# Kernel optimization log

Hardware: AMD Instinct MI355X
Metric: run time of the kernel (lower is better)

The kernel has to match this reference:

```python
import jax, jax.numpy as jnp
import numpy as np
from jax import lax

# Model dims (see init_kwargs / mamba_ssm defaults)
B_, L_, D_IN = 8, 512, 128
D_MODEL, N_LAYERS = 512, 2
EXPAND, D_STATE, D_CONV = 2, 16, 4
D_INNER = EXPAND * D_MODEL          # 1024
DT_RANK = (D_MODEL + 15) // 16      # 32


def setup_inputs() -> dict:
    key = jax.random.key(0)
    ks = iter(jax.random.split(key, 32))
    def p(shape, scale=0.02):
        return jax.random.normal(next(ks), shape, jnp.float32) * scale
    inp = {}
    inp["x"] = jax.random.normal(next(ks), (B_, L_, D_IN), jnp.float32)
    # input projection (Linear(input_dim, d_model), with bias)
    inp["proj_in_w"] = p((D_MODEL, D_IN))
    inp["proj_in_b"] = p((D_MODEL,))
    # stacked per-layer Mamba params (leading dim = N_LAYERS)
    inp["in_proj_w"] = p((N_LAYERS, 2 * D_INNER, D_MODEL))      # no bias (mamba default)
    inp["conv_w"]    = p((N_LAYERS, D_INNER, D_CONV))           # depthwise conv1d
    inp["conv_b"]    = p((N_LAYERS, D_INNER))
    inp["x_proj_w"]  = p((N_LAYERS, DT_RANK + 2 * D_STATE, D_INNER))
    inp["dt_proj_w"] = p((N_LAYERS, D_INNER, DT_RANK))
    inp["dt_proj_b"] = jnp.full((N_LAYERS, D_INNER), 0.1, jnp.float32)
    inp["A_log"]     = jnp.log(jnp.tile(jnp.arange(1, D_STATE + 1, dtype=jnp.float32), (N_LAYERS, D_INNER, 1)))
    inp["Dm"]        = jnp.ones((N_LAYERS, D_INNER), jnp.float32)
    inp["out_proj_w"] = p((N_LAYERS, D_MODEL, D_INNER))         # no bias
    # classifier head: Linear(d_model, 64) -> ReLU -> Linear(64, 1)
    inp["cls_w1"] = p((64, D_MODEL)); inp["cls_b1"] = p((64,))
    inp["cls_w2"] = p((1, 64));       inp["cls_b2"] = p((1,))
    return inp


def _mamba_block(h, in_w, cw, cb, xp_w, dt_w, dt_b, A_log, Dm, out_w):
    B, L, _ = h.shape
    xz = jnp.einsum('bld,ed->ble', h, in_w)           # (B, L, 2*d_inner)
    xi, z = jnp.split(xz, 2, axis=-1)
    # causal depthwise conv1d (pad left d_conv-1, crop to L)
    xc = xi.transpose(0, 2, 1)                         # (B, d_inner, L)
    xc = lax.conv_general_dilated(
        xc, cw[:, None, :], (1,), [(D_CONV - 1, 0)],
        feature_group_count=D_INNER,
        dimension_numbers=('NCH', 'OIH', 'NCH')) + cb[None, :, None]
    xc = jax.nn.silu(xc).transpose(0, 2, 1)            # (B, L, d_inner)
    x_dbl = jnp.einsum('bld,ed->ble', xc, xp_w)        # (B, L, dt_rank + 2*d_state)
    dt, Bm, Cm = jnp.split(x_dbl, [DT_RANK, DT_RANK + D_STATE], axis=-1)
    dt = jax.nn.softplus(jnp.einsum('blr,dr->bld', dt, dt_w) + dt_b)  # (B, L, d_inner)
    A = -jnp.exp(A_log)                                # (d_inner, d_state)

    def step(hst, ins):
        dt_t, B_t, C_t, x_t = ins                      # (B,di),(B,ds),(B,ds),(B,di)
        dA = jnp.exp(dt_t[..., None] * A)              # (B, di, ds)
        hst = dA * hst + (dt_t * x_t)[..., None] * B_t[:, None, :]
        y = jnp.einsum('bds,bs->bd', hst, C_t)
        return hst, y

    h0 = jnp.zeros((B, D_INNER, D_STATE), h.dtype)
    xs = (dt.transpose(1, 0, 2), Bm.transpose(1, 0, 2),
          Cm.transpose(1, 0, 2), xc.transpose(1, 0, 2))
    _, ys = lax.scan(step, h0, xs)                     # ys: (L, B, d_inner)
    y = ys.transpose(1, 0, 2) + xc * Dm                # skip term D*x
    y = y * jax.nn.silu(z)                             # gate
    return jnp.einsum('ble,de->bld', y, out_w)         # (B, L, d_model)


def reference(x, proj_in_w, proj_in_b, in_proj_w, conv_w, conv_b, x_proj_w,
              dt_proj_w, dt_proj_b, A_log, Dm, out_proj_w,
              cls_w1, cls_b1, cls_w2, cls_b2):
    h = jnp.einsum('bli,di->bld', x, proj_in_w) + proj_in_b
    for l in range(N_LAYERS):
        h = _mamba_block(h, in_proj_w[l], conv_w[l], conv_b[l], x_proj_w[l],
                         dt_proj_w[l], dt_proj_b[l], A_log[l], Dm[l], out_proj_w[l])
    h = h.mean(axis=1)                                 # (B, d_model); dropout = identity (eval)
    h = jax.nn.relu(h @ cls_w1.T + cls_b1)
    logits = (h @ cls_w2.T + cls_b2).squeeze(-1)       # (B,)
    return logits
```

## Files before the change

### kernel.cpp

```cpp
#include <hip/hip_runtime.h>
#include <hip/hip_bf16.h>

#define B_   8
#define L_   512
#define DIN  128
#define DM   512
#define NLAY 2
#define DI   1024
#define DS   16
#define DTR  32
#define BL   (B_ * L_)
#define KS   8
#define CL   128
#define NCH  (L_ / CL)

typedef short bf16x8 __attribute__((ext_vector_type(8)));
typedef float floatx4 __attribute__((ext_vector_type(4)));

__device__ __forceinline__ unsigned short f2bf(float f) {
    unsigned int u = __float_as_uint(f);
    unsigned int r = (u + 0x7FFF + ((u >> 16) & 1)) >> 16;
    return (unsigned short)r;
}
__device__ __forceinline__ float bf2f(unsigned short u) {
    return __uint_as_float((unsigned int)u << 16);
}

#if __has_builtin(__builtin_amdgcn_exp2f)
#define EXP2(x) __builtin_amdgcn_exp2f(x)
#else
#define EXP2(x) __expf((x) * 0.69314718056f)
#endif

__global__ __launch_bounds__(256) void cvt_all(
    const float* __restrict__ x,  unsigned short* __restrict__ xbf,
    const float* __restrict__ pw, unsigned short* __restrict__ wpin,
    const float* __restrict__ iw, unsigned short* __restrict__ win,
    const float* __restrict__ ow, unsigned short* __restrict__ wout,
    float* __restrict__ hm)
{
    int bid = blockIdx.x;
    if (bid >= 1824) {
        int i = (bid - 1824) * 2048 + threadIdx.x * 8;
        float4 z = make_float4(0.f, 0.f, 0.f, 0.f);
        *(float4*)(hm + i) = z;
        *(float4*)(hm + i + 4) = z;
        return;
    }
    const float* src; unsigned short* dst; int off;
    if      (bid < 256)  { src = x;  dst = xbf;  off = bid; }
    else if (bid < 288)  { src = pw; dst = wpin; off = bid - 256; }
    else if (bid < 1312) { src = iw; dst = win;  off = bid - 288; }
    else                 { src = ow; dst = wout; off = bid - 1312; }
    int i = (off * 256 + threadIdx.x) * 8;
    float4 a = *(const float4*)(src + i);
    float4 b = *(const float4*)(src + i + 4);
    unsigned short o[8];
    o[0] = f2bf(a.x); o[1] = f2bf(a.y); o[2] = f2bf(a.z); o[3] = f2bf(a.w);
    o[4] = f2bf(b.x); o[5] = f2bf(b.y); o[6] = f2bf(b.z); o[7] = f2bf(b.w);
    *(uint4*)(dst + i) = *(uint4*)o;
}

__global__ __launch_bounds__(256) void gemm_mfma(
    const unsigned short* __restrict__ A,
    const unsigned short* __restrict__ W,
    float* __restrict__ C, unsigned short* __restrict__ Cb,
    int N, int K)
{
    __shared__ unsigned short As[128 * 40];
    __shared__ unsigned short Ws[128 * 40];

    const int tid  = threadIdx.x;
    const int row  = tid >> 1;
    const int half = tid & 1;
    const long aBase = (long)(blockIdx.y * 128 + row) * K + half * 16;
    const long wBase = (long)(blockIdx.x * 128 + row) * K + half * 16;
    const int  lbase = row * 40 + half * 16;

    const int lane = tid & 63;
    const int wv   = tid >> 6;
    const int wm   = (wv >> 1) * 64;
    const int wn   = (wv & 1) * 64;
    const int lr   = lane & 15;
    const int q    = lane >> 4;

    floatx4 acc[4][4];
#pragma unroll
    for (int i = 0; i < 4; ++i)
#pragma unroll
        for (int j = 0; j < 4; ++j)
#pragma unroll
            for (int r = 0; r < 4; ++r) acc[i][j][r] = 0.f;

    for (int k0 = 0; k0 < K; k0 += 32) {
        __syncthreads();
        const unsigned short* ap = A + aBase + k0;
        const unsigned short* wp = W + wBase + k0;
        uint4 a0 = *(const uint4*)ap;
        uint4 a1 = *(const uint4*)(ap + 8);
        uint4 w0 = *(const uint4*)wp;
        uint4 w1 = *(const uint4*)(wp + 8);
        *(uint4*)(As + lbase)     = a0;
        *(uint4*)(As + lbase + 8) = a1;
        *(uint4*)(Ws + lbase)     = w0;
        *(uint4*)(Ws + lbase + 8) = w1;
        __syncthreads();

        bf16x8 af[4], bfr[4];
#pragma unroll
        for (int i = 0; i < 4; ++i)
            af[i] = *(const bf16x8*)(As + (wm + i * 16 + lr) * 40 + q * 8);
#pragma unroll
        for (int j = 0; j < 4; ++j)
            bfr[j] = *(const bf16x8*)(Ws + (wn + j * 16 + lr) * 40 + q * 8);
#pragma unroll
        for (int i = 0; i < 4; ++i)
#pragma unroll
            for (int j = 0; j < 4; ++j)
                acc[i][j] = __builtin_amdgcn_mfma_f32_16x16x32_bf16(
                    af[i], bfr[j], acc[i][j], 0, 0, 0);
    }

#pragma unroll
    for (int i = 0; i < 4; ++i) {
#pragma unroll
        for (int r = 0; r < 4; ++r) {
            const int  crow = blockIdx.y * 128 + wm + i * 16 + q * 4 + r;
            const long base = (long)crow * N + blockIdx.x * 128 + wn + lr;
#pragma unroll
            for (int j = 0; j < 4; ++j) {
                float v = acc[i][j][r];
                if (C)  C[base + j * 16] = v;
                if (Cb) Cb[base + j * 16] = f2bf(v);
            }
        }
    }
}

__global__ __launch_bounds__(256) void gemm_mfma_n64(
    const unsigned short* __restrict__ A,
    const unsigned short* __restrict__ W,
    const float* __restrict__ bias,
    float* __restrict__ C, unsigned short* __restrict__ Cb,
    int N, int K, int meanmode, float* __restrict__ hm)
{
    __shared__ unsigned short As[128 * 40];
    __shared__ unsigned short Ws[64 * 40];
    __shared__ float colsum[64];

    const int tid   = threadIdx.x;
    const int arow  = tid >> 1;
    const int ahalf = tid & 1;
    const long aBase = (long)(blockIdx.y * 128 + arow) * K + ahalf * 16;
    const int  albase = arow * 40 + ahalf * 16;
    const int wrow = tid >> 2;
    const int wq   = tid & 3;
    const long wBase = (long)(blockIdx.x * 64 + wrow) * K + wq * 8;
    const int  wlbase = wrow * 40 + wq * 8;

    const int lane = tid & 63;
    const int wv   = tid >> 6;
    const int wm   = wv * 32;
    const int lr   = lane & 15;
    const int q    = lane >> 4;

    floatx4 acc[2][4];
#pragma unroll
    for (int i = 0; i < 2; ++i)
#pragma unroll
        for (int j = 0; j < 4; ++j)
#pragma unroll
            for (int r = 0; r < 4; ++r) acc[i][j][r] = 0.f;

    for (int k0 = 0; k0 < K; k0 += 32) {
        __syncthreads();
        const unsigned short* ap = A + aBase + k0;
        uint4 a0 = *(const uint4*)ap;
        uint4 a1 = *(const uint4*)(ap + 8);
        uint4 w0 = *(const uint4*)(W + wBase + k0);
        *(uint4*)(As + albase)     = a0;
        *(uint4*)(As + albase + 8) = a1;
        *(uint4*)(Ws + wlbase)     = w0;
        __syncthreads();

        bf16x8 af[2], bfr[4];
#pragma unroll
        for (int i = 0; i < 2; ++i)
            af[i] = *(const bf16x8*)(As + (wm + i * 16 + lr) * 40 + q * 8);
#pragma unroll
        for (int j = 0; j < 4; ++j)
            bfr[j] = *(const bf16x8*)(Ws + (j * 16 + lr) * 40 + q * 8);
#pragma unroll
        for (int i = 0; i < 2; ++i)
#pragma unroll
            for (int j = 0; j < 4; ++j)
                acc[i][j] = __builtin_amdgcn_mfma_f32_16x16x32_bf16(
                    af[i], bfr[j], acc[i][j], 0, 0, 0);
    }

    if (meanmode) {
        if (tid < 64) colsum[tid] = 0.f;
        __syncthreads();
#pragma unroll
        for (int j = 0; j < 4; ++j) {
            float p = 0.f;
#pragma unroll
            for (int i = 0; i < 2; ++i)
#pragma unroll
                for (int r = 0; r < 4; ++r) p += acc[i][j][r];
            atomicAdd(&colsum[j * 16 + lr], p);
        }
        __syncthreads();
        if (tid < 64) {
            const int b = blockIdx.y >> 2;
            atomicAdd(&hm[b * DM + blockIdx.x * 64 + tid],
                      colsum[tid] * (1.f / (float)L_));
        }
        return;
    }

    float bj[4] = {0.f, 0.f, 0.f, 0.f};
    if (bias) {
#pragma unroll
        for (int j = 0; j < 4; ++j)
            bj[j] = bias[blockIdx.x * 64 + j * 16 + lr];
    }
#pragma unroll
    for (int i = 0; i < 2; ++i) {
#pragma unroll
        for (int r = 0; r < 4; ++r) {
            const int  crow = blockIdx.y * 128 + wm + i * 16 + q * 4 + r;
            const long base = (long)crow * N + blockIdx.x * 64 + lr;
#pragma unroll
            for (int j = 0; j < 4; ++j) {
                float v = acc[i][j][r] + bj[j];
                if (C)  C[base + j * 16] = v;
                if (Cb) Cb[base + j * 16] = f2bf(v);
            }
        }
    }
}

__global__ __launch_bounds__(256) void xprojconv(
    const unsigned short* __restrict__ xzb, const float* __restrict__ cw,
    const float* __restrict__ cb, const float* __restrict__ W,
    float* __restrict__ P, float* __restrict__ xcout)
{
    __shared__ float As[16][68];
    __shared__ float Ws[16][68];

    const int tid  = threadIdx.x;
    const int tx   = tid & 15;
    const int ty   = tid >> 4;
    const int lrow = tid >> 2;
    const int lk   = (tid & 3) << 2;
    const int kbase = blockIdx.x * (DI / KS);

    const int m = blockIdx.y * 64 + lrow;
    const int t = m & (L_ - 1);
    const float* Wp = W + lrow * DI + kbase + lk;

    float acc[4][4] = {};

    for (int k0 = 0; k0 < DI / KS; k0 += 16) {
        const int dcol = kbase + k0 + lk;
        float4 cbv = *(const float4*)(cb + dcol);
        float sums[4] = {cbv.x, cbv.y, cbv.z, cbv.w};
        float4 cwq[4];
#pragma unroll
        for (int q = 0; q < 4; ++q) cwq[q] = *(const float4*)(cw + (dcol + q) * 4);
#pragma unroll
        for (int w = 0; w < 4; ++w) {
            int tw = t - 3 + w;
            if (tw >= 0) {
                const uint2 up = *(const uint2*)(xzb + (long)(m - 3 + w) * (2 * DI) + dcol);
                float x0 = __uint_as_float(up.x << 16);
                float x1 = __uint_as_float(up.x & 0xffff0000u);
                float x2 = __uint_as_float(up.y << 16);
                float x3 = __uint_as_float(up.y & 0xffff0000u);
                sums[0] += ((const float*)&cwq[0])[w] * x0;
                sums[1] += ((const float*)&cwq[1])[w] * x1;
                sums[2] += ((const float*)&cwq[2])[w] * x2;
                sums[3] += ((const float*)&cwq[3])[w] * x3;
            }
        }
        float4 a4;
#pragma unroll
        for (int q = 0; q < 4; ++q)
            ((float*)&a4)[q] = sums[q] / (1.f + __expf(-sums[q]));
        float4 wv = *(const float4*)(Wp + k0);
        *(float4*)(xcout + (long)m * DI + dcol) = a4;

        __syncthreads();
        As[lk + 0][lrow] = a4.x; As[lk + 1][lrow] = a4.y;
        As[lk + 2][lrow] = a4.z; As[lk + 3][lrow] = a4.w;
        Ws[lk + 0][lrow] = wv.x; Ws[lk + 1][lrow] = wv.y;
        Ws[lk + 2][lrow] = wv.z; Ws[lk + 3][lrow] = wv.w;
        __syncthreads();
#pragma unroll
        for (int k = 0; k < 16; ++k) {
            const float4 a44 = *(const float4*)&As[k][ty << 2];
            const float4 w4  = *(const float4*)&Ws[k][tx << 2];
            acc[0][0] += a44.x * w4.x; acc[0][1] += a44.x * w4.y;
            acc[0][2] += a44.x * w4.z; acc[0][3] += a44.x * w4.w;
            acc[1][0] += a44.y * w4.x; acc[1][1] += a44.y * w4.y;
            acc[1][2] += a44.y * w4.z; acc[1][3] += a44.y * w4.w;
            acc[2][0] += a44.z * w4.x; acc[2][1] += a44.z * w4.y;
            acc[2][2] += a44.z * w4.z; acc[2][3] += a44.z * w4.w;
            acc[3][0] += a44.w * w4.x; acc[3][1] += a44.w * w4.y;
            acc[3][2] += a44.w * w4.z; acc[3][3] += a44.w * w4.w;
        }
    }

    float* out = P + (long)blockIdx.x * (BL * 64)
               + (blockIdx.y * 64 + (ty << 2)) * 64 + (tx << 2);
#pragma unroll
    for (int i = 0; i < 4; ++i)
        *(float4*)(out + i * 64) = make_float4(acc[i][0], acc[i][1],
                                               acc[i][2], acc[i][3]);
}

__global__ __launch_bounds__(256) void xproj_reduce(
    const float* __restrict__ P, float* __restrict__ xdbl)
{
    int i = (blockIdx.x * 256 + threadIdx.x) * 4;
    float4 s = *(const float4*)(P + i);
#pragma unroll
    for (int k = 1; k < KS; ++k) {
        float4 p = *(const float4*)(P + (long)k * (BL * 64) + i);
        s.x += p.x; s.y += p.y; s.z += p.z; s.w += p.w;
    }
    *(float4*)(xdbl + i) = s;
}

template <int CTRL>
__device__ __forceinline__ float dpp_shr_add(float v) {
    int sh = __builtin_amdgcn_update_dpp(0, __float_as_int(v), CTRL, 0xF, 0xF, true);
    return v + __int_as_float(sh);
}

__global__ __launch_bounds__(256) void scan_fused(
    const float* __restrict__ xc, const float* __restrict__ xdbl,
    const float* __restrict__ A_log, const float* __restrict__ dtw,
    const float* __restrict__ dtpb, const float* __restrict__ Dm,
    const unsigned short* __restrict__ xzb, unsigned short* __restrict__ ysb16)
{
    __shared__ float  sdtw[16][36];
    __shared__ float  sxd [CL][36];
    __shared__ float4 sdp [CL / 2][17];
    __shared__ float4 sbc4[CL / 2][17];
    __shared__ float  sy  [16][CL + 4];

    const int tid  = threadIdx.x;
    const int s    = tid & 15;
    const int grp  = tid >> 4;
    const int bd0  = blockIdx.x * 16;
    const int b    = bd0 >> 10;
    const int d0   = bd0 & (DI - 1);
    const int mb0  = b * L_;

    const int j  = tid & 15;
    const int tt = tid >> 4;

    {
        float2 w = *(const float2*)(dtw + (d0 + j) * DTR + tt * 2);
        sdtw[j][tt * 2] = w.x; sdtw[j][tt * 2 + 1] = w.y;
    }
    const float a    = -__expf(A_log[(d0 + grp) * DS + s]);
    const float bias = dtpb[d0 + j];
    const float dmv  = Dm[d0 + j];

    float  rxc[8], rB[8], rC[8], rz[8];
    float2 rxd[8];
#pragma unroll
    for (int i = 0; i < 8; ++i) {
        int m = mb0 + tt + 16 * i;
        rxc[i] = xc[m * DI + d0 + j];
        rxd[i] = *(const float2*)(xdbl + m * 64 + j * 2);
        rB[i]  = xdbl[m * 64 + DTR + j];
        rC[i]  = xdbl[m * 64 + DTR + DS + j];
        rz[i]  = bf2f(xzb[(long)m * (2 * DI) + DI + d0 + j]);
    }

    float state = 0.f;

    for (int c = 0; c < NCH; ++c) {
        const int mbase = mb0 + c * CL;
        float xcur[8], zcur[8];
#pragma unroll
        for (int i = 0; i < 8; ++i) { xcur[i] = rxc[i]; zcur[i] = rz[i]; }

        __syncthreads();
#pragma unroll
        for (int i = 0; i < 8; ++i) {
            int t = tt + 16 * i;
            *(float2*)&sxd[t][j * 2] = rxd[i];
            ((float2*)&sbc4[t >> 1][j])[t & 1] = make_float2(rB[i], rC[i]);
        }
        __syncthreads();

        if (c < NCH - 1) {
#pragma unroll
            for (int i = 0; i < 8; ++i) {
                int m = mbase + CL + tt + 16 * i;
                rxc[i] = xc[m * DI + d0 + j];
                rxd[i] = *(const float2*)(xdbl + m * 64 + j * 2);
                rB[i]  = xdbl[m * 64 + DTR + j];
                rC[i]  = xdbl[m * 64 + DTR + DS + j];
                rz[i]  = bf2f(xzb[(long)m * (2 * DI) + DI + d0 + j]);
            }
        }

        {
            float4 wreg[8];
#pragma unroll
            for (int k = 0; k < 8; ++k) wreg[k] = *(const float4*)&sdtw[j][k * 4];
#pragma unroll
            for (int i = 0; i < 8; ++i) {
                int t = tt + 16 * i;
                float acc = bias;
#pragma unroll
                for (int k = 0; k < 8; ++k) {
                    float4 xv = *(const float4*)&sxd[t][k * 4];
                    acc += xv.x * wreg[k].x + xv.y * wreg[k].y
                         + xv.z * wreg[k].z + xv.w * wreg[k].w;
                }
                float dt = (acc > 20.f) ? acc : __logf(1.f + __expf(acc));
                ((float2*)&sdp[t >> 1][j])[t & 1] =
                    make_float2(dt * 1.44269504f, dt * xcur[i]);
            }
        }
        __syncthreads();

        for (int t4 = 0; t4 < CL; t4 += 4) {
            float ybuf[4];
#pragma unroll
            for (int h = 0; h < 2; ++h) {
                const int t2 = (t4 >> 1) + h;
                const float4 dp = sdp[t2][grp];
                const float4 bc = sbc4[t2][s];
                {
                    const float dA = EXP2(dp.x * a);
                    state = fmaf(dA, state, dp.y * bc.x);
                    float contrib = state * bc.y;
                    contrib = dpp_shr_add<0x111>(contrib);
                    contrib = dpp_shr_add<0x112>(contrib);
                    contrib = dpp_shr_add<0x114>(contrib);
                    contrib = dpp_shr_add<0x118>(contrib);
                    ybuf[h * 2] = contrib;
                }
                {
                    const float dA = EXP2(dp.z * a);
                    state = fmaf(dA, state, dp.w * bc.z);
                    float contrib = state * bc.w;
                    contrib = dpp_shr_add<0x111>(contrib);
                    contrib = dpp_shr_add<0x112>(contrib);
                    contrib = dpp_shr_add<0x114>(contrib);
                    contrib = dpp_shr_add<0x118>(contrib);
                    ybuf[h * 2 + 1] = contrib;
                }
            }
            if (s == 15) *(float4*)&sy[grp][t4] = *(float4*)ybuf;
        }
        __syncthreads();

#pragma unroll
        for (int i = 0; i < 8; ++i) {
            int t = tt + 16 * i;
            float z = zcur[i];
            float sz = z / (1.f + __expf(-z));
            float val = (sy[j][t] + xcur[i] * dmv) * sz;
            ysb16[(mbase + t) * DI + d0 + j] = f2bf(val);
        }
    }
}

__global__ __launch_bounds__(512) void meancls_kernel(
    const float* __restrict__ hm, const float* __restrict__ w1,
    const float* __restrict__ b1, const float* __restrict__ w2,
    const float* __restrict__ b2, float* __restrict__ out)
{
    __shared__ float shm[DM];
    __shared__ float su[64];
    const int b = blockIdx.x, tid = threadIdx.x;
    shm[tid] = hm[b * DM + tid];
    __syncthreads();

    const int j = tid >> 3, sl = tid & 7;
    const float* wr = w1 + j * DM + sl * 64;
    const float* hb = shm + sl * 64;
    float p = 0.f;
    for (int k = 0; k < 64; k += 4)
        p += hb[k] * wr[k] + hb[k+1] * wr[k+1]
           + hb[k+2] * wr[k+2] + hb[k+3] * wr[k+3];
    p += __shfl_xor(p, 1);
    p += __shfl_xor(p, 2);
    p += __shfl_xor(p, 4);
    if (sl == 0) su[j] = fmaxf(p + b1[j], 0.f) * w2[j];
    __syncthreads();
    if (tid < 64) {
        float v = su[tid];
#pragma unroll
        for (int off = 32; off; off >>= 1) v += __shfl_down(v, off);
        if (tid == 0) out[b] = v + b2[0];
    }
}

extern "C" void kernel_launch(void* const* d_in, const int* in_sizes, int n_in,
                              void* d_out, int out_size, void* d_ws, size_t ws_size,
                              hipStream_t stream) {
    const float* x          = (const float*)d_in[0];
    const float* proj_in_w  = (const float*)d_in[1];
    const float* proj_in_b  = (const float*)d_in[2];
    const float* in_proj_w  = (const float*)d_in[3];
    const float* conv_w     = (const float*)d_in[4];
    const float* conv_b     = (const float*)d_in[5];
    const float* x_proj_w   = (const float*)d_in[6];
    const float* dt_proj_w  = (const float*)d_in[7];
    const float* dt_proj_b  = (const float*)d_in[8];
    const float* A_log      = (const float*)d_in[9];
    const float* Dm         = (const float*)d_in[10];
    const float* out_proj_w = (const float*)d_in[11];
    const float* cls_w1     = (const float*)d_in[12];
    const float* cls_b1     = (const float*)d_in[13];
    const float* cls_w2     = (const float*)d_in[14];
    const float* cls_b2     = (const float*)d_in[15];
    float* out = (float*)d_out;

    float* ws   = (float*)d_ws;
    float* h    = ws;
    float* xzf  = h    + BL * DM;
    float* xcb  = xzf  + BL * 2 * DI;
    float* xdbl = xcb  + BL * DI;
    float* scr  = xdbl + BL * 64;
    float* hm   = scr  + 2 * BL * DI;
    float* hmp  = hm   + B_ * DM;
    unsigned short* xzb  = (unsigned short*)xzf;
    unsigned short* u16  = (unsigned short*)(hmp + 64 * DM);
    unsigned short* xbf  = u16;
    unsigned short* hbf  = xbf  + BL * DIN;
    unsigned short* ysbf = hbf  + BL * DM;
    unsigned short* wpin = ysbf + BL * DI;
    unsigned short* win  = wpin + DM * DIN;
    unsigned short* wout = win  + NLAY * 2 * DI * DM;
    float* xpart = scr;

    cvt_all<<<1826, 256, 0, stream>>>(x, xbf, proj_in_w, wpin,
                                      in_proj_w, win, out_proj_w, wout, hm);

    gemm_mfma_n64<<<dim3(DM / 64, BL / 128), 256, 0, stream>>>(
        xbf, wpin, proj_in_b, nullptr, hbf, DM, DIN, 0, nullptr);

    for (int l = 0; l < NLAY; ++l) {
        gemm_mfma<<<dim3(2 * DI / 128, BL / 128), 256, 0, stream>>>(
            hbf, win + l * 2 * DI * DM, nullptr, xzb, 2 * DI, DM);
        xprojconv<<<dim3(KS, BL / 64), 256, 0, stream>>>(
            xzb, conv_w + l * DI * 4, conv_b + l * DI,
            x_proj_w + l * 64 * DI, xpart, xcb);
        xproj_reduce<<<(BL * 64) / 1024, 256, 0, stream>>>(xpart, xdbl);
        scan_fused<<<(B_ * DI) / 16, 256, 0, stream>>>(
            xcb, xdbl, A_log + l * DI * DS, dt_proj_w + l * DI * DTR,
            dt_proj_b + l * DI, Dm + l * DI, xzb, ysbf);
        if (l == NLAY - 1) {
            gemm_mfma_n64<<<dim3(DM / 64, BL / 128), 256, 0, stream>>>(
                ysbf, wout + l * DM * DI, nullptr, nullptr, nullptr,
                DM, DI, 1, hm);
        } else {
            gemm_mfma_n64<<<dim3(DM / 64, BL / 128), 256, 0, stream>>>(
                ysbf, wout + l * DM * DI, nullptr, nullptr, hbf,
                DM, DI, 0, nullptr);
        }
    }

    meancls_kernel<<<B_, 512, 0, stream>>>(hm, cls_w1, cls_b1,
                                           cls_w2, cls_b2, out);
}
```

Baseline: 347.0 us.

## Fuse classifier into last out-proj GEMM and software-pipeline scan loads

The final out-projection GEMM now ends with a last-block-done counter: the final block to finish reads the accumulated mean and runs the classifier head, which removes a separate kernel launch. The scan kernel keeps the dt_proj weights in registers instead of shared memory. Its inner loop also prefetches the next step's shared-memory operands and computes four state updates before the 16-lane DPP reductions, so reductions overlap the serial recurrence. The cost is a global atomic counter, a serial classifier tail on one block, and higher register pressure in the scan.

```diff
diff --git a/kernel.cpp b/kernel.cpp
--- a/kernel.cpp
+++ b/kernel.cpp
@@ -32,19 +32,33 @@
 #define EXP2(x) __expf((x) * 0.69314718056f)
 #endif
 
-__global__ __launch_bounds__(256) void cvt_all(
+template <int CTRL>
+__device__ __forceinline__ float dpp_shr_add(float v) {
+    int sh = __builtin_amdgcn_update_dpp(0, __float_as_int(v), CTRL, 0xF, 0xF, true);
+    return v + __int_as_float(sh);
+}
+__device__ __forceinline__ float red16(float c) {
+    c = dpp_shr_add<0x111>(c);
+    c = dpp_shr_add<0x112>(c);
+    c = dpp_shr_add<0x114>(c);
+    c = dpp_shr_add<0x118>(c);
+    return c;
+}
+
+__global__ __launch_bounds__(256) void k_cvt(
     const float* __restrict__ x,  unsigned short* __restrict__ xbf,
     const float* __restrict__ pw, unsigned short* __restrict__ wpin,
     const float* __restrict__ iw, unsigned short* __restrict__ win,
     const float* __restrict__ ow, unsigned short* __restrict__ wout,
-    float* __restrict__ hm)
+    float* __restrict__ hm, unsigned int* __restrict__ cnt)
 {
-    int bid = blockIdx.x;
+    int bid = blockIdx.x, tid = threadIdx.x;
     if (bid >= 1824) {
-        int i = (bid - 1824) * 2048 + threadIdx.x * 8;
+        int i = (bid - 1824) * 2048 + tid * 8;
         float4 z = make_float4(0.f, 0.f, 0.f, 0.f);
         *(float4*)(hm + i) = z;
         *(float4*)(hm + i + 4) = z;
+        if (bid == 1825 && tid == 0) cnt[0] = 0u;
         return;
     }
     const float* src; unsigned short* dst; int off;
@@ -52,7 +66,7 @@
     else if (bid < 288)  { src = pw; dst = wpin; off = bid - 256; }
     else if (bid < 1312) { src = iw; dst = win;  off = bid - 288; }
     else                 { src = ow; dst = wout; off = bid - 1312; }
-    int i = (off * 256 + threadIdx.x) * 8;
+    int i = (off * 256 + tid) * 8;
     float4 a = *(const float4*)(src + i);
     float4 b = *(const float4*)(src + i + 4);
     unsigned short o[8];
@@ -61,20 +75,219 @@
     *(uint4*)(dst + i) = *(uint4*)o;
 }
 
-__global__ __launch_bounds__(256) void gemm_mfma(
+__global__ __launch_bounds__(256) void k_gemm_n64(
     const unsigned short* __restrict__ A,
     const unsigned short* __restrict__ W,
-    float* __restrict__ C, unsigned short* __restrict__ Cb,
-    int N, int K)
+    const float* __restrict__ bias,
+    unsigned short* __restrict__ Cb, int K)
+{
+    __shared__ unsigned short As[128 * 40];
+    __shared__ unsigned short Ws[64 * 40];
+
+    const int tid   = threadIdx.x;
+    const int bxx   = blockIdx.x, byy = blockIdx.y;
+    const int arow  = tid >> 1;
+    const int ahalf = tid & 1;
+    const long aBase = (long)(byy * 128 + arow) * K + ahalf * 16;
+    const int  albase = arow * 40 + ahalf * 16;
+    const int wrow = tid >> 2;
+    const int wq   = tid & 3;
+    const long wBase = (long)(bxx * 64 + wrow) * K + wq * 8;
+    const int  wlbase = wrow * 40 + wq * 8;
+
+    const int lane = tid & 63;
+    const int wv   = tid >> 6;
+    const int wm   = wv * 32;
+    const int lr   = lane & 15;
+    const int q    = lane >> 4;
+
+    floatx4 acc[2][4];
+#pragma unroll
+    for (int i = 0; i < 2; ++i)
+#pragma unroll
+        for (int j = 0; j < 4; ++j)
+#pragma unroll
+            for (int r = 0; r < 4; ++r) acc[i][j][r] = 0.f;
+
+    for (int k0 = 0; k0 < K; k0 += 32) {
+        __syncthreads();
+        const unsigned short* ap = A + aBase + k0;
+        uint4 a0 = *(const uint4*)ap;
+        uint4 a1 = *(const uint4*)(ap + 8);
+        uint4 w0 = *(const uint4*)(W + wBase + k0);
+        *(uint4*)(As + albase)     = a0;
+        *(uint4*)(As + albase + 8) = a1;
+        *(uint4*)(Ws + wlbase)     = w0;
+        __syncthreads();
+
+        bf16x8 af[2], bfr[4];
+#pragma unroll
+        for (int i = 0; i < 2; ++i)
+            af[i] = *(const bf16x8*)(As + (wm + i * 16 + lr) * 40 + q * 8);
+#pragma unroll
+        for (int j = 0; j < 4; ++j)
+            bfr[j] = *(const bf16x8*)(Ws + (j * 16 + lr) * 40 + q * 8);
+#pragma unroll
+        for (int i = 0; i < 2; ++i)
+#pragma unroll
+            for (int j = 0; j < 4; ++j)
+                acc[i][j] = __builtin_amdgcn_mfma_f32_16x16x32_bf16(
+                    af[i], bfr[j], acc[i][j], 0, 0, 0);
+    }
+
+    float bj[4] = {0.f, 0.f, 0.f, 0.f};
+    if (bias) {
+#pragma unroll
+        for (int j = 0; j < 4; ++j)
+            bj[j] = bias[bxx * 64 + j * 16 + lr];
+    }
+#pragma unroll
+    for (int i = 0; i < 2; ++i) {
+#pragma unroll
+        for (int r = 0; r < 4; ++r) {
+            const int  crow = byy * 128 + wm + i * 16 + q * 4 + r;
+            const long base = (long)crow * DM + bxx * 64 + lr;
+#pragma unroll
+            for (int j = 0; j < 4; ++j)
+                Cb[base + j * 16] = f2bf(acc[i][j][r] + bj[j]);
+        }
+    }
+}
+
+__global__ __launch_bounds__(256) void k_outproj_cls(
+    const unsigned short* __restrict__ A,
+    const unsigned short* __restrict__ W,
+    float* __restrict__ hm, unsigned int* __restrict__ cnt,
+    const float* __restrict__ w1, const float* __restrict__ b1,
+    const float* __restrict__ w2, const float* __restrict__ b2,
+    float* __restrict__ out)
+{
+    __shared__ unsigned short As[128 * 40];
+    __shared__ unsigned short Ws[64 * 40];
+    __shared__ float colsum[64];
+    __shared__ int last;
+
+    const int tid = threadIdx.x;
+    const int bxx = blockIdx.x, byy = blockIdx.y;
+    const int K = DI;
+    const int arow  = tid >> 1;
+    const int ahalf = tid & 1;
+    const long aBase = (long)(byy * 128 + arow) * K + ahalf * 16;
+    const int  albase = arow * 40 + ahalf * 16;
+    const int wrow = tid >> 2;
+    const int wq   = tid & 3;
+    const long wBase = (long)(bxx * 64 + wrow) * K + wq * 8;
+    const int  wlbase = wrow * 40 + wq * 8;
+
+    const int lane = tid & 63;
+    const int wv   = tid >> 6;
+    const int wm   = wv * 32;
+    const int lr   = lane & 15;
+    const int q    = lane >> 4;
+
+    floatx4 acc[2][4];
+#pragma unroll
+    for (int i = 0; i < 2; ++i)
+#pragma unroll
+        for (int j = 0; j < 4; ++j)
+#pragma unroll
+            for (int r = 0; r < 4; ++r) acc[i][j][r] = 0.f;
+
+    for (int k0 = 0; k0 < K; k0 += 32) {
+        __syncthreads();
+        const unsigned short* ap = A + aBase + k0;
+        uint4 a0 = *(const uint4*)ap;
+        uint4 a1 = *(const uint4*)(ap + 8);
+        uint4 w0 = *(const uint4*)(W + wBase + k0);
+        *(uint4*)(As + albase)     = a0;
+        *(uint4*)(As + albase + 8) = a1;
+        *(uint4*)(Ws + wlbase)     = w0;
+        __syncthreads();
+
+        bf16x8 af[2], bfr[4];
+#pragma unroll
+        for (int i = 0; i < 2; ++i)
+            af[i] = *(const bf16x8*)(As + (wm + i * 16 + lr) * 40 + q * 8);
+#pragma unroll
+        for (int j = 0; j < 4; ++j)
+            bfr[j] = *(const bf16x8*)(Ws + (j * 16 + lr) * 40 + q * 8);
+#pragma unroll
+        for (int i = 0; i < 2; ++i)
+#pragma unroll
+            for (int j = 0; j < 4; ++j)
+                acc[i][j] = __builtin_amdgcn_mfma_f32_16x16x32_bf16(
+                    af[i], bfr[j], acc[i][j], 0, 0, 0);
+    }
+
+    __syncthreads();
+    if (tid < 64) colsum[tid] = 0.f;
+    __syncthreads();
+#pragma unroll
+    for (int j = 0; j < 4; ++j) {
+        float pp = 0.f;
+#pragma unroll
+        for (int i = 0; i < 2; ++i)
+#pragma unroll
+            for (int r = 0; r < 4; ++r) pp += acc[i][j][r];
+        atomicAdd(&colsum[j * 16 + lr], pp);
+    }
+    __syncthreads();
+    if (tid < 64) {
+        const int b = byy >> 2;
+        atomicAdd(&hm[b * DM + bxx * 64 + tid],
+                  colsum[tid] * (1.f / (float)L_));
+    }
+    __syncthreads();
+
+    if (tid == 0) {
+        __threadfence();
+        unsigned int old = atomicAdd(cnt, 1u);
+        last = (old == 255u) ? 1 : 0;
+    }
+    __syncthreads();
+    if (!last) return;
+
+    float* shm = (float*)As;
+    float* su  = (float*)Ws;
+    for (int b = 0; b < B_; ++b) {
+        shm[tid]       = atomicAdd(&hm[b * DM + tid], 0.f);
+        shm[tid + 256] = atomicAdd(&hm[b * DM + tid + 256], 0.f);
+        __syncthreads();
+        const int jj = tid >> 2, sl = tid & 3;
+        const float* wr = w1 + jj * DM + sl * 128;
+        const float* hb = shm + sl * 128;
+        float pp = 0.f;
+        for (int k = 0; k < 128; k += 4)
+            pp += hb[k] * wr[k] + hb[k+1] * wr[k+1]
+                + hb[k+2] * wr[k+2] + hb[k+3] * wr[k+3];
+        pp += __shfl_xor(pp, 1);
+        pp += __shfl_xor(pp, 2);
+        if (sl == 0) su[jj] = fmaxf(pp + b1[jj], 0.f) * w2[jj];
+        __syncthreads();
+        if (tid < 64) {
+            float v = su[tid];
+#pragma unroll
+            for (int off = 32; off; off >>= 1) v += __shfl_down(v, off);
+            if (tid == 0) out[b] = v + b2[0];
+        }
+        __syncthreads();
+    }
+}
+
+__global__ __launch_bounds__(256) void k_gemm_128(
+    const unsigned short* __restrict__ A,
+    const unsigned short* __restrict__ W,
+    unsigned short* __restrict__ Cb, int N, int K)
 {
     __shared__ unsigned short As[128 * 40];
     __shared__ unsigned short Ws[128 * 40];
 
     const int tid  = threadIdx.x;
+    const int bxx  = blockIdx.x, byy = blockIdx.y;
     const int row  = tid >> 1;
     const int half = tid & 1;
-    const long aBase = (long)(blockIdx.y * 128 + row) * K + half * 16;
-    const long wBase = (long)(blockIdx.x * 128 + row) * K + half * 16;
+    const long aBase = (long)(byy * 128 + row) * K + half * 16;
+    const long wBase = (long)(bxx * 128 + row) * K + half * 16;
     const int  lbase = row * 40 + half * 16;
 
     const int lane = tid & 63;
@@ -125,123 +338,16 @@
     for (int i = 0; i < 4; ++i) {
 #pragma unroll
         for (int r = 0; r < 4; ++r) {
-            const int  crow = blockIdx.y * 128 + wm + i * 16 + q * 4 + r;
-            const long base = (long)crow * N + blockIdx.x * 128 + wn + lr;
-#pragma unroll
-            for (int j = 0; j < 4; ++j) {
-                float v = acc[i][j][r];
-                if (C)  C[base + j * 16] = v;
-                if (Cb) Cb[base + j * 16] = f2bf(v);
-            }
-        }
-    }
-}
-
-__global__ __launch_bounds__(256) void gemm_mfma_n64(
-    const unsigned short* __restrict__ A,
-    const unsigned short* __restrict__ W,
-    const float* __restrict__ bias,
-    float* __restrict__ C, unsigned short* __restrict__ Cb,
-    int N, int K, int meanmode, float* __restrict__ hm)
-{
-    __shared__ unsigned short As[128 * 40];
-    __shared__ unsigned short Ws[64 * 40];
-    __shared__ float colsum[64];
-
-    const int tid   = threadIdx.x;
-    const int arow  = tid >> 1;
-    const int ahalf = tid & 1;
-    const long aBase = (long)(blockIdx.y * 128 + arow) * K + ahalf * 16;
-    const int  albase = arow * 40 + ahalf * 16;
-    const int wrow = tid >> 2;
-    const int wq   = tid & 3;
-    const long wBase = (long)(blockIdx.x * 64 + wrow) * K + wq * 8;
-    const int  wlbase = wrow * 40 + wq * 8;
-
-    const int lane = tid & 63;
-    const int wv   = tid >> 6;
-    const int wm   = wv * 32;
-    const int lr   = lane & 15;
-    const int q    = lane >> 4;
-
-    floatx4 acc[2][4];
-#pragma unroll
-    for (int i = 0; i < 2; ++i)
-#pragma unroll
-        for (int j = 0; j < 4; ++j)
-#pragma unroll
-            for (int r = 0; r < 4; ++r) acc[i][j][r] = 0.f;
-
-    for (int k0 = 0; k0 < K; k0 += 32) {
-        __syncthreads();
-        const unsigned short* ap = A + aBase + k0;
-        uint4 a0 = *(const uint4*)ap;
-        uint4 a1 = *(const uint4*)(ap + 8);
-        uint4 w0 = *(const uint4*)(W + wBase + k0);
-        *(uint4*)(As + albase)     = a0;
-        *(uint4*)(As + albase + 8) = a1;
-        *(uint4*)(Ws + wlbase)     = w0;
-        __syncthreads();
-
-        bf16x8 af[2], bfr[4];
-#pragma unroll
-        for (int i = 0; i < 2; ++i)
-            af[i] = *(const bf16x8*)(As + (wm + i * 16 + lr) * 40 + q * 8);
-#pragma unroll
-        for (int j = 0; j < 4; ++j)
-            bfr[j] = *(const bf16x8*)(Ws + (j * 16 + lr) * 40 + q * 8);
-#pragma unroll
-        for (int i = 0; i < 2; ++i)
+            const int  crow = byy * 128 + wm + i * 16 + q * 4 + r;
+            const long base = (long)crow * N + bxx * 128 + wn + lr;
 #pragma unroll
             for (int j = 0; j < 4; ++j)
-                acc[i][j] = __builtin_amdgcn_mfma_f32_16x16x32_bf16(
-                    af[i], bfr[j], acc[i][j], 0, 0, 0);
-    }
-
-    if (meanmode) {
-        if (tid < 64) colsum[tid] = 0.f;
-        __syncthreads();
-#pragma unroll
-        for (int j = 0; j < 4; ++j) {
-            float p = 0.f;
-#pragma unroll
-            for (int i = 0; i < 2; ++i)
-#pragma unroll
-                for (int r = 0; r < 4; ++r) p += acc[i][j][r];
-            atomicAdd(&colsum[j * 16 + lr], p);
-        }
-        __syncthreads();
-        if (tid < 64) {
-            const int b = blockIdx.y >> 2;
-            atomicAdd(&hm[b * DM + blockIdx.x * 64 + tid],
-                      colsum[tid] * (1.f / (float)L_));
-        }
-        return;
-    }
-
-    float bj[4] = {0.f, 0.f, 0.f, 0.f};
-    if (bias) {
-#pragma unroll
-        for (int j = 0; j < 4; ++j)
-            bj[j] = bias[blockIdx.x * 64 + j * 16 + lr];
-    }
-#pragma unroll
-    for (int i = 0; i < 2; ++i) {
-#pragma unroll
-        for (int r = 0; r < 4; ++r) {
-            const int  crow = blockIdx.y * 128 + wm + i * 16 + q * 4 + r;
-            const long base = (long)crow * N + blockIdx.x * 64 + lr;
-#pragma unroll
-            for (int j = 0; j < 4; ++j) {
-                float v = acc[i][j][r] + bj[j];
-                if (C)  C[base + j * 16] = v;
-                if (Cb) Cb[base + j * 16] = f2bf(v);
-            }
-        }
-    }
-}
-
-__global__ __launch_bounds__(256) void xprojconv(
+                Cb[base + j * 16] = f2bf(acc[i][j][r]);
+        }
+    }
+}
+
+__global__ __launch_bounds__(256) void k_xprojconv(
     const unsigned short* __restrict__ xzb, const float* __restrict__ cw,
     const float* __restrict__ cb, const float* __restrict__ W,
     float* __restrict__ P, float* __restrict__ xcout)
@@ -268,7 +374,7 @@
         float sums[4] = {cbv.x, cbv.y, cbv.z, cbv.w};
         float4 cwq[4];
 #pragma unroll
-        for (int q = 0; q < 4; ++q) cwq[q] = *(const float4*)(cw + (dcol + q) * 4);
+        for (int qq = 0; qq < 4; ++qq) cwq[qq] = *(const float4*)(cw + (dcol + qq) * 4);
 #pragma unroll
         for (int w = 0; w < 4; ++w) {
             int tw = t - 3 + w;
@@ -286,8 +392,8 @@
         }
         float4 a4;
 #pragma unroll
-        for (int q = 0; q < 4; ++q)
-            ((float*)&a4)[q] = sums[q] / (1.f + __expf(-sums[q]));
+        for (int qq = 0; qq < 4; ++qq)
+            ((float*)&a4)[qq] = sums[qq] / (1.f + __expf(-sums[qq]));
         float4 wv = *(const float4*)(Wp + k0);
         *(float4*)(xcout + (long)m * DI + dcol) = a4;
 
@@ -312,40 +418,33 @@
         }
     }
 
-    float* out = P + (long)blockIdx.x * (BL * 64)
-               + (blockIdx.y * 64 + (ty << 2)) * 64 + (tx << 2);
+    float* outp = P + (long)blockIdx.x * (BL * 64)
+                + (blockIdx.y * 64 + (ty << 2)) * 64 + (tx << 2);
 #pragma unroll
     for (int i = 0; i < 4; ++i)
-        *(float4*)(out + i * 64) = make_float4(acc[i][0], acc[i][1],
-                                               acc[i][2], acc[i][3]);
-}
-
-__global__ __launch_bounds__(256) void xproj_reduce(
+        *(float4*)(outp + i * 64) = make_float4(acc[i][0], acc[i][1],
+                                                acc[i][2], acc[i][3]);
+}
+
+__global__ __launch_bounds__(256) void k_reduce(
     const float* __restrict__ P, float* __restrict__ xdbl)
 {
     int i = (blockIdx.x * 256 + threadIdx.x) * 4;
     float4 s = *(const float4*)(P + i);
 #pragma unroll
     for (int k = 1; k < KS; ++k) {
-        float4 p = *(const float4*)(P + (long)k * (BL * 64) + i);
-        s.x += p.x; s.y += p.y; s.z += p.z; s.w += p.w;
+        float4 pp = *(const float4*)(P + (long)k * (BL * 64) + i);
+        s.x += pp.x; s.y += pp.y; s.z += pp.z; s.w += pp.w;
     }
     *(float4*)(xdbl + i) = s;
 }
 
-template <int CTRL>
-__device__ __forceinline__ float dpp_shr_add(float v) {
-    int sh = __builtin_amdgcn_update_dpp(0, __float_as_int(v), CTRL, 0xF, 0xF, true);
-    return v + __int_as_float(sh);
-}
-
-__global__ __launch_bounds__(256) void scan_fused(
+__global__ __launch_bounds__(256) void k_scan(
     const float* __restrict__ xc, const float* __restrict__ xdbl,
     const float* __restrict__ A_log, const float* __restrict__ dtw,
     const float* __restrict__ dtpb, const float* __restrict__ Dm,
     const unsigned short* __restrict__ xzb, unsigned short* __restrict__ ysb16)
 {
-    __shared__ float  sdtw[16][36];
     __shared__ float  sxd [CL][36];
     __shared__ float4 sdp [CL / 2][17];
     __shared__ float4 sbc4[CL / 2][17];
@@ -362,13 +461,13 @@
     const int j  = tid & 15;
     const int tt = tid >> 4;
 
-    {
-        float2 w = *(const float2*)(dtw + (d0 + j) * DTR + tt * 2);
-        sdtw[j][tt * 2] = w.x; sdtw[j][tt * 2 + 1] = w.y;
-    }
     const float a    = -__expf(A_log[(d0 + grp) * DS + s]);
     const float bias = dtpb[d0 + j];
     const float dmv  = Dm[d0 + j];
+    float4 wreg[8];
+#pragma unroll
+    for (int k = 0; k < 8; ++k)
+        wreg[k] = *(const float4*)(dtw + (d0 + j) * DTR + k * 4);
 
     float  rxc[8], rB[8], rC[8], rz[8];
     float2 rxd[8];
@@ -411,55 +510,42 @@
             }
         }
 
-        {
-            float4 wreg[8];
-#pragma unroll
-            for (int k = 0; k < 8; ++k) wreg[k] = *(const float4*)&sdtw[j][k * 4];
-#pragma unroll
-            for (int i = 0; i < 8; ++i) {
-                int t = tt + 16 * i;
-                float acc = bias;
-#pragma unroll
-                for (int k = 0; k < 8; ++k) {
-                    float4 xv = *(const float4*)&sxd[t][k * 4];
-                    acc += xv.x * wreg[k].x + xv.y * wreg[k].y
-                         + xv.z * wreg[k].z + xv.w * wreg[k].w;
-                }
-                float dt = (acc > 20.f) ? acc : __logf(1.f + __expf(acc));
-                ((float2*)&sdp[t >> 1][j])[t & 1] =
-                    make_float2(dt * 1.44269504f, dt * xcur[i]);
+#pragma unroll
+        for (int i = 0; i < 8; ++i) {
+            int t = tt + 16 * i;
+            float acc = bias;
+#pragma unroll
+            for (int k = 0; k < 8; ++k) {
+                float4 xv = *(const float4*)&sxd[t][k * 4];
+                acc += xv.x * wreg[k].x + xv.y * wreg[k].y
+                     + xv.z * wreg[k].z + xv.w * wreg[k].w;
             }
-        }
-        __syncthreads();
-
+            float dt = (acc > 20.f) ? acc : __logf(1.f + __expf(acc));
+            ((float2*)&sdp[t >> 1][j])[t & 1] =
+                make_float2(dt * 1.44269504f, dt * xcur[i]);
+        }
+        __syncthreads();
+
+        float4 dp0 = sdp[0][grp], dp1 = sdp[1][grp];
+        float4 bc0 = sbc4[0][s],  bc1 = sbc4[1][s];
         for (int t4 = 0; t4 < CL; t4 += 4) {
+            const float4 cd0 = dp0, cd1 = dp1, cb0 = bc0, cb1 = bc1;
+            if (t4 + 4 < CL) {
+                const int t2 = (t4 >> 1) + 2;
+                dp0 = sdp[t2][grp];     dp1 = sdp[t2 + 1][grp];
+                bc0 = sbc4[t2][s];      bc1 = sbc4[t2 + 1][s];
+            }
+            const float dA0 = EXP2(cd0.x * a), dA1 = EXP2(cd0.z * a);
+            const float dA2 = EXP2(cd1.x * a), dA3 = EXP2(cd1.z * a);
+            const float u0 = cd0.y * cb0.x, u1 = cd0.w * cb0.z;
+            const float u2 = cd1.y * cb1.x, u3 = cd1.w * cb1.z;
+            state = fmaf(dA0, state, u0); float c0 = state * cb0.y;
+            state = fmaf(dA1, state, u1); float c1 = state * cb0.w;
+            state = fmaf(dA2, state, u2); float c2 = state * cb1.y;
+            state = fmaf(dA3, state, u3); float c3 = state * cb1.w;
             float ybuf[4];
-#pragma unroll
-            for (int h = 0; h < 2; ++h) {
-                const int t2 = (t4 >> 1) + h;
-                const float4 dp = sdp[t2][grp];
-                const float4 bc = sbc4[t2][s];
-                {
-                    const float dA = EXP2(dp.x * a);
-                    state = fmaf(dA, state, dp.y * bc.x);
-                    float contrib = state * bc.y;
-                    contrib = dpp_shr_add<0x111>(contrib);
-                    contrib = dpp_shr_add<0x112>(contrib);
-                    contrib = dpp_shr_add<0x114>(contrib);
-                    contrib = dpp_shr_add<0x118>(contrib);
-                    ybuf[h * 2] = contrib;
-                }
-                {
-                    const float dA = EXP2(dp.z * a);
-                    state = fmaf(dA, state, dp.w * bc.z);
-                    float contrib = state * bc.w;
-                    contrib = dpp_shr_add<0x111>(contrib);
-                    contrib = dpp_shr_add<0x112>(contrib);
-                    contrib = dpp_shr_add<0x114>(contrib);
-                    contrib = dpp_shr_add<0x118>(contrib);
-                    ybuf[h * 2 + 1] = contrib;
-                }
-            }
+            ybuf[0] = red16(c0); ybuf[1] = red16(c1);
+            ybuf[2] = red16(c2); ybuf[3] = red16(c3);
             if (s == 15) *(float4*)&sy[grp][t4] = *(float4*)ybuf;
         }
         __syncthreads();
@@ -472,37 +558,6 @@
             float val = (sy[j][t] + xcur[i] * dmv) * sz;
             ysb16[(mbase + t) * DI + d0 + j] = f2bf(val);
         }
-    }
-}
-
-__global__ __launch_bounds__(512) void meancls_kernel(
-    const float* __restrict__ hm, const float* __restrict__ w1,
-    const float* __restrict__ b1, const float* __restrict__ w2,
-    const float* __restrict__ b2, float* __restrict__ out)
-{
-    __shared__ float shm[DM];
-    __shared__ float su[64];
-    const int b = blockIdx.x, tid = threadIdx.x;
-    shm[tid] = hm[b * DM + tid];
-    __syncthreads();
-
-    const int j = tid >> 3, sl = tid & 7;
-    const float* wr = w1 + j * DM + sl * 64;
-    const float* hb = shm + sl * 64;
-    float p = 0.f;
-    for (int k = 0; k < 64; k += 4)
-        p += hb[k] * wr[k] + hb[k+1] * wr[k+1]
-           + hb[k+2] * wr[k+2] + hb[k+3] * wr[k+3];
-    p += __shfl_xor(p, 1);
-    p += __shfl_xor(p, 2);
-    p += __shfl_xor(p, 4);
-    if (sl == 0) su[j] = fmaxf(p + b1[j], 0.f) * w2[j];
-    __syncthreads();
-    if (tid < 64) {
-        float v = su[tid];
-#pragma unroll
-        for (int off = 32; off; off >>= 1) v += __shfl_down(v, off);
-        if (tid == 0) out[b] = v + b2[0];
     }
 }
 
@@ -534,44 +589,41 @@
     float* xdbl = xcb  + BL * DI;
     float* scr  = xdbl + BL * 64;
     float* hm   = scr  + 2 * BL * DI;
-    float* hmp  = hm   + B_ * DM;
-    unsigned short* xzb  = (unsigned short*)xzf;
-    unsigned short* u16  = (unsigned short*)(hmp + 64 * DM);
+    unsigned int* cnt = (unsigned int*)(hm + B_ * DM);
+    float* hmp  = hm + B_ * DM;
+    float* xpart = scr;
+
+    unsigned short* xzb = (unsigned short*)xzf;
+    unsigned short* u16 = (unsigned short*)(hmp + 64 * DM);
     unsigned short* xbf  = u16;
     unsigned short* hbf  = xbf  + BL * DIN;
     unsigned short* ysbf = hbf  + BL * DM;
     unsigned short* wpin = ysbf + BL * DI;
     unsigned short* win  = wpin + DM * DIN;
     unsigned short* wout = win  + NLAY * 2 * DI * DM;
-    float* xpart = scr;
-
-    cvt_all<<<1826, 256, 0, stream>>>(x, xbf, proj_in_w, wpin,
-                                      in_proj_w, win, out_proj_w, wout, hm);
-
-    gemm_mfma_n64<<<dim3(DM / 64, BL / 128), 256, 0, stream>>>(
-        xbf, wpin, proj_in_b, nullptr, hbf, DM, DIN, 0, nullptr);
+
+    k_cvt<<<1826, 256, 0, stream>>>(x, xbf, proj_in_w, wpin, in_proj_w, win,
+                                    out_proj_w, wout, hm, cnt);
+
+    k_gemm_n64<<<dim3(8, 32), 256, 0, stream>>>(xbf, wpin, proj_in_b, hbf, DIN);
 
     for (int l = 0; l < NLAY; ++l) {
-        gemm_mfma<<<dim3(2 * DI / 128, BL / 128), 256, 0, stream>>>(
-            hbf, win + l * 2 * DI * DM, nullptr, xzb, 2 * DI, DM);
-        xprojconv<<<dim3(KS, BL / 64), 256, 0, stream>>>(
+        k_gemm_128<<<dim3(16, 32), 256, 0, stream>>>(
+            hbf, win + l * 2 * DI * DM, xzb, 2 * DI, DM);
+        k_xprojconv<<<dim3(KS, 64), 256, 0, stream>>>(
             xzb, conv_w + l * DI * 4, conv_b + l * DI,
             x_proj_w + l * 64 * DI, xpart, xcb);
-        xproj_reduce<<<(BL * 64) / 1024, 256, 0, stream>>>(xpart, xdbl);
-        scan_fused<<<(B_ * DI) / 16, 256, 0, stream>>>(
+        k_reduce<<<256, 256, 0, stream>>>(xpart, xdbl);
+        k_scan<<<512, 256, 0, stream>>>(
             xcb, xdbl, A_log + l * DI * DS, dt_proj_w + l * DI * DTR,
             dt_proj_b + l * DI, Dm + l * DI, xzb, ysbf);
         if (l == NLAY - 1) {
-            gemm_mfma_n64<<<dim3(DM / 64, BL / 128), 256, 0, stream>>>(
-                ysbf, wout + l * DM * DI, nullptr, nullptr, nullptr,
-                DM, DI, 1, hm);
+            k_outproj_cls<<<dim3(8, 32), 256, 0, stream>>>(
+                ysbf, wout + l * DM * DI, hm, cnt,
+                cls_w1, cls_b1, cls_w2, cls_b2, out);
         } else {
-            gemm_mfma_n64<<<dim3(DM / 64, BL / 128), 256, 0, stream>>>(
-                ysbf, wout + l * DM * DI, nullptr, nullptr, hbf,
-                DM, DI, 0, nullptr);
-        }
-    }
-
-    meancls_kernel<<<B_, 512, 0, stream>>>(hm, cls_w1, cls_b1,
-                                           cls_w2, cls_b2, out);
-}
+            k_gemm_n64<<<dim3(8, 32), 256, 0, stream>>>(
+                ysbf, wout + l * DM * DI, nullptr, hbf, DI);
+        }
+    }
+}
```

After: 374.8 us. 8.0% more time.
